# Kernel tuning notes

Measured on AMD Instinct MI355X. Metric: run time of the kernel, lower is better.

## Reference

```python
import jax, jax.numpy as jnp
import numpy as np

B, C, H, W = 2, 16, 128, 128
PS = (3, 5, 7)
N_BG, N_TG = 64, 8


def _unfold(x, p):
    # torch F.unfold(kernel=p, padding=p//2, stride=1): [B,C,H,W] -> [B, C*p*p, H*W]
    pad = p // 2
    b, c, h, w = x.shape
    xp = jnp.pad(x, ((0, 0), (0, 0), (pad, pad), (pad, pad)))
    # channel-major, then kernel row, kernel col (torch layout)
    pat = jnp.stack([xp[:, :, i:i + h, j:j + w] for i in range(p) for j in range(p)], axis=2)
    return pat.reshape(b, c * p * p, h * w)


def _fold(cols, p, h, w):
    # torch F.fold(output_size=(h,w), kernel=p, padding=p//2, stride=1): overlap-add scatter
    b, d, _ = cols.shape
    c = d // (p * p)
    pad = p // 2
    pat = cols.reshape(b, c, p * p, h, w)
    canvas = jnp.zeros((b, c, h + 2 * pad, w + 2 * pad), cols.dtype)
    for k in range(p * p):
        i, j = divmod(k, p)
        canvas = canvas.at[:, :, i:i + h, j:j + w].add(pat[:, :, k])
    return canvas[:, :, pad:pad + h, pad:pad + w]


def _branch(x, memory, temp, p):
    # _read_memory ('dot' similarity) + fold reconstruction with overlap-count divisor
    b, c, h, w = x.shape
    d = memory.shape[1]  # c*p*p
    xu = _unfold(x, p).transpose(0, 2, 1)                      # [B, HW, D]
    sim = jnp.einsum('bld,md->blm', xu, memory) * (temp[0] / d ** 0.5)
    att = jax.nn.softmax(sim, axis=2)                          # [B, HW, M]
    read = jnp.einsum('blm,md->bld', att, memory)              # [B, HW, D]
    out_sum = _fold(read.transpose(0, 2, 1), p, h, w)
    ones = jnp.ones((1, 1, h, w), x.dtype)
    div = _fold(_unfold(ones, p), p, h, w)                     # overlap counts
    return out_sum / (div + 1e-8)


def _fusion(feats, w1, b1, w2, b2):
    # MultiScaleFusion, fusion_type='attention'
    n = len(feats)
    b, c = feats[0].shape[0], feats[0].shape[1]
    u = feats[0]
    for f in feats[1:]:
        u = u + f
    pooled = u.mean(axis=(2, 3))                               # [B, C]
    hdn = jax.nn.relu(pooled @ w1.T + b1)                      # [B, C//4]
    logits = (hdn @ w2.T + b2).reshape(b, n, c)                # [B, n, C]
    wt = jax.nn.softmax(logits, axis=1)[..., None, None]       # softmax over scales
    return (jnp.stack(feats, axis=1) * wt).sum(axis=1)


def setup_inputs() -> dict:
    key = jax.random.key(0)
    ks = jax.random.split(key, 20)
    inp = {
        'bg': jax.random.normal(ks[0], (B, C, H, W), jnp.float32),
        'tg': jax.random.normal(ks[1], (B, C, H, W), jnp.float32),
    }
    for i, p in enumerate(PS):
        inp[f'bg_mem{i}'] = jax.random.normal(ks[2 + i], (N_BG, C * p * p), jnp.float32)
        inp[f'tg_mem{i}'] = jax.random.normal(ks[5 + i], (N_TG, C * p * p), jnp.float32)
        inp[f'bg_temp{i}'] = jnp.full((1,), 10.0, jnp.float32)
        inp[f'tg_temp{i}'] = jnp.full((1,), 10.0, jnp.float32)
    hid = C // 4
    n = len(PS)
    s1 = (1.0 / C) ** 0.5
    s2 = (1.0 / hid) ** 0.5
    inp['bg_fc1_w'] = jax.random.uniform(ks[8], (hid, C), jnp.float32, -s1, s1)
    inp['bg_fc1_b'] = jax.random.uniform(ks[9], (hid,), jnp.float32, -s1, s1)
    inp['bg_fc2_w'] = jax.random.uniform(ks[10], (C * n, hid), jnp.float32, -s2, s2)
    inp['bg_fc2_b'] = jax.random.uniform(ks[11], (C * n,), jnp.float32, -s2, s2)
    inp['tg_fc1_w'] = jax.random.uniform(ks[12], (hid, C), jnp.float32, -s1, s1)
    inp['tg_fc1_b'] = jax.random.uniform(ks[13], (hid,), jnp.float32, -s1, s1)
    inp['tg_fc2_w'] = jax.random.uniform(ks[14], (C * n, hid), jnp.float32, -s2, s2)
    inp['tg_fc2_b'] = jax.random.uniform(ks[15], (C * n,), jnp.float32, -s2, s2)
    return inp


def reference(bg, tg,
              bg_mem0, bg_mem1, bg_mem2, bg_temp0, bg_temp1, bg_temp2,
              tg_mem0, tg_mem1, tg_mem2, tg_temp0, tg_temp1, tg_temp2,
              bg_fc1_w, bg_fc1_b, bg_fc2_w, bg_fc2_b,
              tg_fc1_w, tg_fc1_b, tg_fc2_w, tg_fc2_b):
    bg_feats = [_branch(bg, m, t, p) for m, t, p in
                zip((bg_mem0, bg_mem1, bg_mem2), (bg_temp0, bg_temp1, bg_temp2), PS)]
    f_bc = _fusion(bg_feats, bg_fc1_w, bg_fc1_b, bg_fc2_w, bg_fc2_b)
    tg_feats = [_branch(tg, m, t, p) for m, t, p in
                zip((tg_mem0, tg_mem1, tg_mem2), (tg_temp0, tg_temp1, tg_temp2), PS)]
    f_tg = _fusion(tg_feats, tg_fc1_w, tg_fc1_b, tg_fc2_w, tg_fc2_b)
    return (f_bc, f_tg)
```

## Files before the change

### kernel.cpp

```cpp
#include <hip/hip_runtime.h>

#define C_CH 16
#define Hdim 128
#define Wdim 128
#define HWdim 16384
#define CHW (C_CH * HWdim)
#define Bdim 2
#define PAIR_ELEMS (Bdim * CHW)

#define XWP 140
#define XHP 140
#define XPL (XHP * XWP)

typedef float v2f __attribute__((ext_vector_type(2)));
typedef _Float16 h2 __attribute__((ext_vector_type(2)));
typedef _Float16 f16x8 __attribute__((ext_vector_type(8)));
typedef float f32x4 __attribute__((ext_vector_type(4)));

__device__ __forceinline__ unsigned pack2(float a, float b) {
  h2 h = {(_Float16)a, (_Float16)b};
  return __builtin_bit_cast(unsigned, h);
}
__device__ __forceinline__ void gadd(float* p, float v) {
  __hip_atomic_fetch_add(p, v, __ATOMIC_RELAXED, __HIP_MEMORY_SCOPE_AGENT);
}

struct PrepDesc {
  const float* mem;
  const float* temp;
  _Float16* simA;
  _Float16* readA;
  int M, D, P, tg;
};
struct PrepArgs { PrepDesc d[6]; };

__global__ __launch_bounds__(256) void k_prep(PrepArgs a) {
  PrepDesc de = a.d[blockIdx.y];
  int n = de.M * de.D;
  int idx = blockIdx.x * 256 + threadIdx.x;
  if (idx >= n) return;
  int m = idx / de.D;
  int d = idx - m * de.D;
  float val = de.mem[idx];
  float sc = de.temp[0] / sqrtf((float)de.D);
  int pp = de.P * de.P;
  int c = d / pp;
  int r = d - c * pp;
  int i = r / de.P;
  int j = r - i * de.P;
  int uv = i * de.P + j;
  int uvp = uv >> 1, luv = uv & 1;
  int kk = luv * 16 + c, kg = kk >> 3, kl = kk & 7;
  int u = de.P - 1 - i, v = de.P - 1 - j;
  int uvf = u * de.P + v;
  float sv = val * sc;
  if (!de.tg) {
    int mt = m >> 4, row = m & 15;
    _Float16 hi = (_Float16)sv;
    size_t bi = ((size_t)uvp * 8 + mt) * 512 + row * 32 +
                (size_t)((kg ^ (row & 3)) * 8 + kl);
    de.simA[bi] = hi;
    de.simA[bi + 2048] = (_Float16)(sv - (float)hi);
    int ck = m >> 5, m5 = m & 31, kg2 = m5 >> 3, kl2 = m5 & 7;
    _Float16 hr = (_Float16)val;
    size_t b2 = (size_t)uvf * 2048 + (size_t)(ck * 2) * 512 + c * 32 +
                (size_t)((kg2 ^ (c & 3)) * 8 + kl2);
    de.readA[b2] = hr;
    de.readA[b2 + 512] = (_Float16)(val - (float)hr);
  } else {
    _Float16 hi = (_Float16)sv;
    size_t bi = (size_t)(uvp * 2) * 512 + m * 32 +
                (size_t)((kg ^ (m & 3)) * 8 + kl);
    de.simA[bi] = hi;
    de.simA[bi + 512] = (_Float16)(sv - (float)hi);
    int ch = uvf >> 2, q = uvf & 3;
    _Float16 hr = (_Float16)val;
    size_t b2 = (size_t)ch * 1024 + c * 32 +
                (size_t)((q ^ (c & 3)) * 8 + (m & 7));
    de.readA[b2] = hr;
    de.readA[b2 + 512] = (_Float16)(val - (float)hr);
  }
}

__global__ __launch_bounds__(256) void k_padx(const float* __restrict__ bg,
                                              const float* __restrict__ tg,
                                              unsigned* __restrict__ xpad2)
{
  int idx = blockIdx.x * 256 + threadIdx.x;
  int pp = idx >> 14;
  int hw = idx & (HWdim - 1);
  int y = hw >> 7, x = hw & 127;
  int z = pp >> 3, cp = pp & 7;
  const float* src = (z < 2) ? bg : tg;
  int b = z & 1;
  float a = src[((b * C_CH + 2 * cp) << 14) + hw];
  float bb = src[((b * C_CH + 2 * cp + 1) << 14) + hw];
  xpad2[(size_t)pp * XPL + (y + 6) * XWP + (x + 6)] = pack2(a, bb);
}

struct FusedArgs {
  const unsigned* xpad2;
  const _Float16* simA[3];
  const _Float16* readA[3];
  const _Float16* simAtg[3];
  const _Float16* readAtg[3];
  float* fbgs[3];
  float* ftgs[3];
  float* pooled;
};

#define FX_ATT 17920
#define FX_ABUF 58880
#define FX_SMEM 75264

template<int P, bool BG>
__device__ __forceinline__ void fused_body(
    const unsigned* __restrict__ xp,
    const _Float16* __restrict__ simA,
    const _Float16* __restrict__ readA,
    float* __restrict__ fout,
    float* __restrict__ poolp,
    unsigned char* smem, int tid, int x0, int y0)
{
  constexpr int PAD = P / 2;
  constexpr int THY = 8 + 2 * PAD, THX = 16 + 2 * PAD;
  constexpr int XH = 8 + 4 * PAD, XW = 16 + 4 * PAD;
  constexpr int NXP = XH * XW, NHP = THY * THX;
  constexpr int NT = (NHP + 15) / 16;
  constexpr int NUVP = (P * P + 1) / 2;
  constexpr int NCH = BG ? (P * P + 1) / 2 : (P * P + 3) / 4;
  constexpr int NMT = BG ? 4 : 1;
  constexpr int SCHB = BG ? 8192 : 2048;
  constexpr int RCHB = BG ? 8192 : 2048;
  constexpr int SLD = SCHB / 16, RLD = RCHB / 16;
  constexpr int NRACC = BG ? 4 : 2;

  unsigned char* xbuf = smem;
  unsigned char* att  = smem + FX_ATT;
  unsigned char* abuf = smem + FX_ABUF;

  const int w = __builtin_amdgcn_readfirstlane(tid >> 6);
  const int lane = tid & 63;
  const int col = lane & 15, g = lane >> 4;

  const int oy = y0 - 2 * PAD + 6, ox = x0 - 2 * PAD + 6;
  for (int t = tid; t < 2 * NXP; t += 512) {
    int h = (t >= NXP) ? 1 : 0;
    int pix = t - h * NXP;
    int ly = pix / XW, lx = pix - ly * XW;
    const unsigned* s = xp + (size_t)(h * 4) * XPL + (oy + ly) * XWP + (ox + lx);
    uint4 vv = { s[0], s[XPL], s[2 * XPL], s[3 * XPL] };
    *(uint4*)(xbuf + (h * NXP + pix) * 16) = vv;
  }

  int ayv[3], axv[3];
#pragma unroll
  for (int ti = 0; ti < 3; ++ti) {
    int nt = w + ti * 8;
    int pix = nt * 16 + col;
    if (pix > NHP - 1) pix = NHP - 1;
    ayv[ti] = pix / THX;
    axv[ti] = pix - ayv[ti] * THX;
  }

  f32x4 acc[3][NMT];
#pragma unroll
  for (int ti = 0; ti < 3; ++ti)
#pragma unroll
    for (int mt = 0; mt < NMT; ++mt) acc[ti][mt] = (f32x4){0.f, 0.f, 0.f, 0.f};

  uint4 sreg;
  if (tid < SLD) sreg = *((const uint4*)simA + tid);
  for (int uvp = 0; uvp < NUVP; ++uvp) {
    if (tid < SLD) {
      *((uint4*)(abuf + (uvp & 1) * 8192) + tid) = sreg;
      if (uvp + 1 < NUVP)
        sreg = *((const uint4*)(simA + (size_t)(uvp + 1) * (SCHB / 2)) + tid);
    }
    __syncthreads();

    const unsigned char* ab = abuf + (uvp & 1) * 8192;
    f16x8 af[2][NMT];
#pragma unroll
    for (int s = 0; s < 2; ++s)
#pragma unroll
      for (int mt = 0; mt < NMT; ++mt)
        af[s][mt] = *(const f16x8*)(ab + (s * NMT + mt) * 1024 + col * 64 +
                                    ((g ^ (col & 3)) << 4));

    int uva = 2 * uvp;
    int uvb = uva + 1; if (uvb >= P * P) uvb = uva;
    const int ua = uva / P, va = uva - ua * P;
    const int ub = uvb / P, vb = uvb - ub * P;
    const int u_ = (g >= 2) ? ub : ua;
    const int v_ = (g >= 2) ? vb : va;

#pragma unroll
    for (int ti = 0; ti < 3; ++ti) {
      int nt = w + ti * 8;
      if (nt < NT) {
        int xpix = (ayv[ti] + u_) * XW + axv[ti] + v_;
        f16x8 bb = *(const f16x8*)(xbuf + ((g & 1) * NXP + xpix) * 16);
#pragma unroll
        for (int mt = 0; mt < NMT; ++mt) {
          acc[ti][mt] = __builtin_amdgcn_mfma_f32_16x16x32_f16(af[0][mt], bb, acc[ti][mt], 0, 0, 0);
          acc[ti][mt] = __builtin_amdgcn_mfma_f32_16x16x32_f16(af[1][mt], bb, acc[ti][mt], 0, 0, 0);
        }
      }
    }
  }

  uint4 rreg;
  if (tid < RLD) rreg = *((const uint4*)readA + tid);

#pragma unroll
  for (int ti = 0; ti < 3; ++ti) {
    int nt = w + ti * 8;
    if (nt < NT) {
      int pa = nt * 16 + col;
      int say = pa / THX, sax = pa - say * THX;
      int gy = y0 + say - PAD, gx = x0 + sax - PAD;
      bool inimg = (pa < NHP) & (gy >= 0) & (gy < Hdim) & (gx >= 0) & (gx < Wdim);
      if constexpr (BG) {
        float l[16];
#pragma unroll
        for (int mt = 0; mt < 4; ++mt)
#pragma unroll
          for (int r = 0; r < 4; ++r) l[mt * 4 + r] = acc[ti][mt][r];
        float mx = l[0];
#pragma unroll
        for (int i2 = 1; i2 < 16; ++i2) mx = fmaxf(mx, l[i2]);
        mx = fmaxf(mx, __shfl_xor(mx, 16));
        mx = fmaxf(mx, __shfl_xor(mx, 32));
        float sum = 0.f;
#pragma unroll
        for (int i2 = 0; i2 < 16; ++i2) { l[i2] = __expf(l[i2] - mx); sum += l[i2]; }
        sum += __shfl_xor(sum, 16);
        sum += __shfl_xor(sum, 32);
        float inv = inimg ? (1.f / sum) : 0.f;
        unsigned char* base = att + pa * 128;
        int swz = (pa & 7) << 4;
#pragma unroll
        for (int mt = 0; mt < 4; ++mt) {
          uint2 st = { pack2(l[mt * 4 + 0] * inv, l[mt * 4 + 1] * inv),
                       pack2(l[mt * 4 + 2] * inv, l[mt * 4 + 3] * inv) };
          *(uint2*)(base + ((mt * 32 + g * 8) ^ swz)) = st;
        }
      } else {
        float l0 = acc[ti][0][0], l1 = acc[ti][0][1];
        float l2 = acc[ti][0][2], l3 = acc[ti][0][3];
        float mx = fmaxf(fmaxf(l0, l1), fmaxf(l2, l3));
        mx = fmaxf(mx, __shfl_xor(mx, 16));
        l0 = __expf(l0 - mx); l1 = __expf(l1 - mx);
        l2 = __expf(l2 - mx); l3 = __expf(l3 - mx);
        float sum = l0 + l1 + l2 + l3;
        sum += __shfl_xor(sum, 16);
        float inv = inimg ? (1.f / sum) : 0.f;
        if (g < 2) {
          uint2 st = { pack2(l0 * inv, l1 * inv), pack2(l2 * inv, l3 * inv) };
          *(uint2*)(att + pa * 16 + g * 8) = st;
        }
      }
    }
  }
  __syncthreads();

  f32x4 racc[NRACC];
#pragma unroll
  for (int q = 0; q < NRACC; ++q) racc[q] = (f32x4){0.f, 0.f, 0.f, 0.f};

  for (int ch = 0; ch < NCH; ++ch) {
    if (tid < RLD) {
      *((uint4*)(abuf + (ch & 1) * 8192) + tid) = rreg;
      if (ch + 1 < NCH)
        rreg = *((const uint4*)(readA + (size_t)(ch + 1) * (RCHB / 2)) + tid);
    }
    __syncthreads();
    const unsigned char* ab = abuf + (ch & 1) * 8192;
    if constexpr (BG) {
#pragma unroll
      for (int l = 0; l < 2; ++l) {
        int uv = 2 * ch + l;
        int uvc = (uv > P * P - 1) ? (P * P - 1) : uv;
        int u = uvc / P, v = uvc - u * P;
        int pix = (w + u) * THX + (col + v);
        int swz = (pix & 7) << 4;
#pragma unroll
        for (int ck = 0; ck < 2; ++ck) {
          f16x8 bb = *(const f16x8*)(att + pix * 128 + ((ck * 64 + g * 16) ^ swz));
          f16x8 ah = *(const f16x8*)(ab + (l * 4 + ck * 2 + 0) * 1024 + col * 64 +
                                     ((g ^ (col & 3)) << 4));
          f16x8 al = *(const f16x8*)(ab + (l * 4 + ck * 2 + 1) * 1024 + col * 64 +
                                     ((g ^ (col & 3)) << 4));
          racc[ck * 2 + 0] = __builtin_amdgcn_mfma_f32_16x16x32_f16(ah, bb, racc[ck * 2 + 0], 0, 0, 0);
          racc[ck * 2 + 1] = __builtin_amdgcn_mfma_f32_16x16x32_f16(al, bb, racc[ck * 2 + 1], 0, 0, 0);
        }
      }
    } else {
      int uv = 4 * ch + g;
      if (uv > P * P - 1) uv = P * P - 1;
      int u = uv / P, v = uv - u * P;
      int pix = (w + u) * THX + (col + v);
      f16x8 bb = *(const f16x8*)(att + pix * 16);
      int aoff = col * 64 + ((g ^ (col & 3)) << 4);
      f16x8 ah = *(const f16x8*)(ab + aoff);
      f16x8 al = *(const f16x8*)(ab + 1024 + aoff);
      racc[0] = __builtin_amdgcn_mfma_f32_16x16x32_f16(ah, bb, racc[0], 0, 0, 0);
      racc[1] = __builtin_amdgcn_mfma_f32_16x16x32_f16(al, bb, racc[1], 0, 0, 0);
    }
  }

  f32x4 sv;
  if constexpr (BG) sv = (racc[0] + racc[1]) + (racc[2] + racc[3]);
  else              sv = racc[0] + racc[1];
  int gy = y0 + w, gx = x0 + col;
  int cy = min(P - 1, gy + PAD) - max(0, gy + PAD - (Hdim - 1)) + 1;
  int cx = min(P - 1, gx + PAD) - max(0, gx + PAD - (Wdim - 1)) + 1;
  float inv = 1.f / ((float)(cy * cx) + 1e-8f);
  float o0 = sv[0] * inv, o1 = sv[1] * inv, o2 = sv[2] * inv, o3 = sv[3] * inv;
  float* outp = fout + (size_t)(g * 4) * HWdim + gy * Wdim + gx;
  outp[0] = o0;
  outp[(size_t)1 * HWdim] = o1;
  outp[(size_t)2 * HWdim] = o2;
  outp[(size_t)3 * HWdim] = o3;

  __syncthreads();
  *(f32x4*)(abuf + tid * 16) = (f32x4){o0, o1, o2, o3};
  __syncthreads();
  if (tid < 16) {
    const float* ap = (const float*)abuf;
    float sum = 0.f;
    for (int px = 0; px < 128; ++px) {
      int u = (px >> 4) * 64 + (tid >> 2) * 16 + (px & 15);
      sum += ap[u * 4 + (tid & 3)];
    }
    gadd(poolp + tid, sum * (1.0f / (float)HWdim));
  }
}

__global__ __launch_bounds__(512, 4) void k_fused(FusedArgs a) {
  __shared__ __align__(16) unsigned char smem[FX_SMEM];
  const int z = blockIdx.z;
  const int x0 = blockIdx.x * 16, y0 = blockIdx.y * 8;
  const int tid = threadIdx.x;
  if (z < 6) {
    const int si = z >> 1, b = z & 1;
    const unsigned* xp = a.xpad2 + (size_t)(b * 8) * XPL;
    float* pp = a.pooled + b * 16;
    if (si == 0)
      fused_body<7, true>(xp, a.simA[0], a.readA[0], a.fbgs[0] + (size_t)b * CHW, pp, smem, tid, x0, y0);
    else if (si == 1)
      fused_body<5, true>(xp, a.simA[1], a.readA[1], a.fbgs[1] + (size_t)b * CHW, pp, smem, tid, x0, y0);
    else
      fused_body<3, true>(xp, a.simA[2], a.readA[2], a.fbgs[2] + (size_t)b * CHW, pp, smem, tid, x0, y0);
  } else {
    const int zz = z - 6, si = zz >> 1, b = zz & 1;
    const unsigned* xp = a.xpad2 + (size_t)((2 + b) * 8) * XPL;
    float* pp = a.pooled + 32 + b * 16;
    if (si == 0)
      fused_body<7, false>(xp, a.simAtg[0], a.readAtg[0], a.ftgs[0] + (size_t)b * CHW, pp, smem, tid, x0, y0);
    else if (si == 1)
      fused_body<5, false>(xp, a.simAtg[1], a.readAtg[1], a.ftgs[1] + (size_t)b * CHW, pp, smem, tid, x0, y0);
    else
      fused_body<3, false>(xp, a.simAtg[2], a.readAtg[2], a.ftgs[2] + (size_t)b * CHW, pp, smem, tid, x0, y0);
  }
}

__global__ __launch_bounds__(128) void k_mlp(
    const float* __restrict__ pooled,
    const float* __restrict__ w1b, const float* __restrict__ b1b,
    const float* __restrict__ w2b, const float* __restrict__ b2b,
    const float* __restrict__ w1t, const float* __restrict__ b1t,
    const float* __restrict__ w2t, const float* __restrict__ b2t,
    float* __restrict__ wt)
{
  __shared__ float hdn[Bdim][4];
  __shared__ float lg[Bdim][48];
  int t = threadIdx.x;
  for (int br = 0; br < 2; ++br) {
    const float* w1 = br ? w1t : w1b;
    const float* b1 = br ? b1t : b1b;
    const float* w2 = br ? w2t : w2b;
    const float* b2 = br ? b2t : b2b;
    if (t < 8) {
      int b = t >> 2, h = t & 3;
      float s = b1[h];
      for (int c = 0; c < C_CH; ++c) s += pooled[br * 32 + b * 16 + c] * w1[h * 16 + c];
      hdn[b][h] = fmaxf(s, 0.f);
    }
    __syncthreads();
    if (t < 96) {
      int b = t / 48, j = t - b * 48;
      float s = b2[j];
      for (int h = 0; h < 4; ++h) s += hdn[b][h] * w2[j * 4 + h];
      lg[b][j] = s;
    }
    __syncthreads();
    if (t < 32) {
      int b = t >> 4, c = t & 15;
      float l0 = lg[b][c], l1 = lg[b][16 + c], l2 = lg[b][32 + c];
      float m = fmaxf(l0, fmaxf(l1, l2));
      float e0 = __expf(l0 - m), e1 = __expf(l1 - m), e2 = __expf(l2 - m);
      float inv = 1.f / (e0 + e1 + e2);
      wt[((br * 2 + b) * 3 + 0) * 16 + c] = e0 * inv;
      wt[((br * 2 + b) * 3 + 1) * 16 + c] = e1 * inv;
      wt[((br * 2 + b) * 3 + 2) * 16 + c] = e2 * inv;
    }
    __syncthreads();
  }
}

__global__ __launch_bounds__(256) void k_out(const float* __restrict__ fbg,
                                             const float* __restrict__ ftg,
                                             const float* __restrict__ wt,
                                             float* __restrict__ out)
{
  int idx = blockIdx.x * 256 + threadIdx.x;
  int br  = idx >> 19;
  int rem = idx & ((1 << 19) - 1);
  int b   = rem >> 18;
  int off = rem & ((1 << 18) - 1);
  int c   = off >> 14;
  const float* f = (br == 0) ? fbg : ftg;
  int wbase = (br * 2 + b) * 3;
  float acc = 0.f;
#pragma unroll
  for (int s = 0; s < 3; ++s) {
    float v = f[(size_t)(s * 2 + b) * CHW + off];
    acc = fmaf(wt[(wbase + s) * 16 + c], v, acc);
  }
  out[idx] = acc;
}

extern "C" void kernel_launch(void* const* d_in, const int* in_sizes, int n_in,
                              void* d_out, int out_size, void* d_ws, size_t ws_size,
                              hipStream_t stream)
{
  const float* bg = (const float*)d_in[0];
  const float* tg = (const float*)d_in[1];
  const float* bg_mem[3]  = {(const float*)d_in[2],  (const float*)d_in[6],  (const float*)d_in[10]};
  const float* tg_mem[3]  = {(const float*)d_in[3],  (const float*)d_in[7],  (const float*)d_in[11]};
  const float* bg_temp[3] = {(const float*)d_in[4],  (const float*)d_in[8],  (const float*)d_in[12]};
  const float* tg_temp[3] = {(const float*)d_in[5],  (const float*)d_in[9],  (const float*)d_in[13]};
  const float* bg_fc1_w = (const float*)d_in[14];
  const float* bg_fc1_b = (const float*)d_in[15];
  const float* bg_fc2_w = (const float*)d_in[16];
  const float* bg_fc2_b = (const float*)d_in[17];
  const float* tg_fc1_w = (const float*)d_in[18];
  const float* tg_fc1_b = (const float*)d_in[19];
  const float* tg_fc2_w = (const float*)d_in[20];
  const float* tg_fc2_b = (const float*)d_in[21];

  unsigned* ws = (unsigned*)d_ws;
  unsigned* xpad2   = ws;
  float*    pooled  = (float*)(ws + (size_t)32 * XPL);
  float*    wt      = pooled + 64;
  _Float16* simA    = (_Float16*)(wt + 192);
  _Float16* readA   = simA + 176128;
  _Float16* simAtg  = readA + 176128;
  _Float16* readAtg = simAtg + 44032;
  float*    ftg     = (float*)(readAtg + 23552);
  float*    fbg     = ftg + (size_t)6 * CHW;

  hipMemsetAsync(xpad2, 0, (size_t)837376 * 4, stream);

  const int   Ms[6] = {64, 64, 64, 8, 8, 8};
  const int   Ps[6] = {3, 5, 7, 3, 5, 7};
  const float* mems[6]  = {bg_mem[0], bg_mem[1], bg_mem[2], tg_mem[0], tg_mem[1], tg_mem[2]};
  const float* temps[6] = {bg_temp[0], bg_temp[1], bg_temp[2], tg_temp[0], tg_temp[1], tg_temp[2]};

  const size_t aOff[3]   = {0, 102400, 155648};
  const size_t sOffTg[3] = {0, 25600, 38912};
  const size_t rOffTg[3] = {0, 13312, 20480};

  PrepArgs pa;
  for (int k = 0; k < 6; ++k) {
    int D = C_CH * Ps[k] * Ps[k];
    int si = 2 - (k % 3);
    if (k < 3)
      pa.d[k] = {mems[k], temps[k], simA + aOff[si], readA + aOff[si],
                 Ms[k], D, Ps[k], 0};
    else
      pa.d[k] = {mems[k], temps[k], simAtg + sOffTg[si], readAtg + rOffTg[si],
                 Ms[k], D, Ps[k], 1};
  }
  k_prep<<<dim3(196, 6), 256, 0, stream>>>(pa);
  k_padx<<<2048, 256, 0, stream>>>(bg, tg, xpad2);

  FusedArgs fa;
  fa.xpad2 = xpad2;
  fa.pooled = pooled;
  for (int si = 0; si < 3; ++si) {
    int p = 2 - si;
    fa.simA[si]    = simA + aOff[si];
    fa.readA[si]   = readA + aOff[si];
    fa.simAtg[si]  = simAtg + sOffTg[si];
    fa.readAtg[si] = readAtg + rOffTg[si];
    fa.fbgs[si]    = fbg + (size_t)p * 2 * CHW;
    fa.ftgs[si]    = ftg + (size_t)p * 2 * CHW;
  }

  k_fused<<<dim3(8, 16, 12), 512, 0, stream>>>(fa);

  k_mlp<<<1, 128, 0, stream>>>(pooled, bg_fc1_w, bg_fc1_b, bg_fc2_w, bg_fc2_b,
                               tg_fc1_w, tg_fc1_b, tg_fc2_w, tg_fc2_b, wt);
  k_out<<<(2 * PAIR_ELEMS) / 256, 256, 0, stream>>>(fbg, ftg, wt, (float*)d_out);
}
```

Measured before the change: 177.0 us.

## Shrink fused-kernel LDS footprint for higher occupancy and merge prep/pad launches

```diff
diff --git a/kernel.cpp b/kernel.cpp
--- a/kernel.cpp
+++ b/kernel.cpp
@@ -34,10 +34,30 @@
 };
 struct PrepArgs { PrepDesc d[6]; };
 
-__global__ __launch_bounds__(256) void k_prep(PrepArgs a) {
-  PrepDesc de = a.d[blockIdx.y];
+__global__ __launch_bounds__(256) void k_preppad(PrepArgs a,
+                                                 const float* __restrict__ bg,
+                                                 const float* __restrict__ tg,
+                                                 unsigned* __restrict__ xpad2)
+{
+  int bid = blockIdx.x;
+  if (bid < 2048) {
+    int idx = bid * 256 + threadIdx.x;
+    int pp = idx >> 14;
+    int hw = idx & (HWdim - 1);
+    int y = hw >> 7, x = hw & 127;
+    int z = pp >> 3, cp = pp & 7;
+    const float* src = (z < 2) ? bg : tg;
+    int b = z & 1;
+    float av = src[((b * C_CH + 2 * cp) << 14) + hw];
+    float bv = src[((b * C_CH + 2 * cp + 1) << 14) + hw];
+    xpad2[(size_t)pp * XPL + (y + 6) * XWP + (x + 6)] = pack2(av, bv);
+    return;
+  }
+  int p = bid - 2048;
+  int gy = p / 196, gx = p - gy * 196;
+  PrepDesc de = a.d[gy];
   int n = de.M * de.D;
-  int idx = blockIdx.x * 256 + threadIdx.x;
+  int idx = gx * 256 + threadIdx.x;
   if (idx >= n) return;
   int m = idx / de.D;
   int d = idx - m * de.D;
@@ -82,22 +102,6 @@
   }
 }
 
-__global__ __launch_bounds__(256) void k_padx(const float* __restrict__ bg,
-                                              const float* __restrict__ tg,
-                                              unsigned* __restrict__ xpad2)
-{
-  int idx = blockIdx.x * 256 + threadIdx.x;
-  int pp = idx >> 14;
-  int hw = idx & (HWdim - 1);
-  int y = hw >> 7, x = hw & 127;
-  int z = pp >> 3, cp = pp & 7;
-  const float* src = (z < 2) ? bg : tg;
-  int b = z & 1;
-  float a = src[((b * C_CH + 2 * cp) << 14) + hw];
-  float bb = src[((b * C_CH + 2 * cp + 1) << 14) + hw];
-  xpad2[(size_t)pp * XPL + (y + 6) * XWP + (x + 6)] = pack2(a, bb);
-}
-
 struct FusedArgs {
   const unsigned* xpad2;
   const _Float16* simA[3];
@@ -109,9 +113,9 @@
   float* pooled;
 };
 
-#define FX_ATT 17920
-#define FX_ABUF 58880
-#define FX_SMEM 75264
+#define SDB_OFF 17920
+#define RBUF_OFF 40960
+#define FX_SMEM 49152
 
 template<int P, bool BG>
 __device__ __forceinline__ void fused_body(
@@ -136,8 +140,9 @@
   constexpr int NRACC = BG ? 4 : 2;
 
   unsigned char* xbuf = smem;
-  unsigned char* att  = smem + FX_ATT;
-  unsigned char* abuf = smem + FX_ABUF;
+  unsigned char* att  = smem;
+  unsigned char* sdb  = smem + SDB_OFF;
+  unsigned char* rbuf = smem + RBUF_OFF;
 
   const int w = __builtin_amdgcn_readfirstlane(tid >> 6);
   const int lane = tid & 63;
@@ -173,13 +178,13 @@
   if (tid < SLD) sreg = *((const uint4*)simA + tid);
   for (int uvp = 0; uvp < NUVP; ++uvp) {
     if (tid < SLD) {
-      *((uint4*)(abuf + (uvp & 1) * 8192) + tid) = sreg;
+      *((uint4*)(sdb + (uvp & 1) * SCHB) + tid) = sreg;
       if (uvp + 1 < NUVP)
         sreg = *((const uint4*)(simA + (size_t)(uvp + 1) * (SCHB / 2)) + tid);
     }
     __syncthreads();
 
-    const unsigned char* ab = abuf + (uvp & 1) * 8192;
+    const unsigned char* ab = sdb + (uvp & 1) * SCHB;
     f16x8 af[2][NMT];
 #pragma unroll
     for (int s = 0; s < 2; ++s)
@@ -212,6 +217,7 @@
 
   uint4 rreg;
   if (tid < RLD) rreg = *((const uint4*)readA + tid);
+  __syncthreads();
 
 #pragma unroll
   for (int ti = 0; ti < 3; ++ti) {
@@ -263,20 +269,20 @@
       }
     }
   }
-  __syncthreads();
 
   f32x4 racc[NRACC];
 #pragma unroll
   for (int q = 0; q < NRACC; ++q) racc[q] = (f32x4){0.f, 0.f, 0.f, 0.f};
 
   for (int ch = 0; ch < NCH; ++ch) {
+    __syncthreads();
     if (tid < RLD) {
-      *((uint4*)(abuf + (ch & 1) * 8192) + tid) = rreg;
+      *((uint4*)rbuf + tid) = rreg;
       if (ch + 1 < NCH)
         rreg = *((const uint4*)(readA + (size_t)(ch + 1) * (RCHB / 2)) + tid);
     }
     __syncthreads();
-    const unsigned char* ab = abuf + (ch & 1) * 8192;
+    const unsigned char* ab = rbuf;
     if constexpr (BG) {
 #pragma unroll
       for (int l = 0; l < 2; ++l) {
@@ -324,21 +330,32 @@
   outp[(size_t)2 * HWdim] = o2;
   outp[(size_t)3 * HWdim] = o3;
 
+  float s0 = o0, s1 = o1, s2 = o2, s3 = o3;
+#pragma unroll
+  for (int mask = 1; mask < 16; mask <<= 1) {
+    s0 += __shfl_xor(s0, mask);
+    s1 += __shfl_xor(s1, mask);
+    s2 += __shfl_xor(s2, mask);
+    s3 += __shfl_xor(s3, mask);
+  }
   __syncthreads();
-  *(f32x4*)(abuf + tid * 16) = (f32x4){o0, o1, o2, o3};
+  float* red = (float*)rbuf;
+  if (col == 0) {
+    red[(w * 4 + g) * 4 + 0] = s0;
+    red[(w * 4 + g) * 4 + 1] = s1;
+    red[(w * 4 + g) * 4 + 2] = s2;
+    red[(w * 4 + g) * 4 + 3] = s3;
+  }
   __syncthreads();
   if (tid < 16) {
-    const float* ap = (const float*)abuf;
-    float sum = 0.f;
-    for (int px = 0; px < 128; ++px) {
-      int u = (px >> 4) * 64 + (tid >> 2) * 16 + (px & 15);
-      sum += ap[u * 4 + (tid & 3)];
-    }
-    gadd(poolp + tid, sum * (1.0f / (float)HWdim));
-  }
-}
-
-__global__ __launch_bounds__(512, 4) void k_fused(FusedArgs a) {
+    float t = 0.f;
+#pragma unroll
+    for (int ww = 0; ww < 8; ++ww) t += red[ww * 16 + tid];
+    gadd(poolp + tid, t * (1.0f / (float)HWdim));
+  }
+}
+
+__global__ __launch_bounds__(512, 6) void k_fused(FusedArgs a) {
   __shared__ __align__(16) unsigned char smem[FX_SMEM];
   const int z = blockIdx.z;
   const int x0 = blockIdx.x * 16, y0 = blockIdx.y * 8;
@@ -484,8 +501,7 @@
       pa.d[k] = {mems[k], temps[k], simAtg + sOffTg[si], readAtg + rOffTg[si],
                  Ms[k], D, Ps[k], 1};
   }
-  k_prep<<<dim3(196, 6), 256, 0, stream>>>(pa);
-  k_padx<<<2048, 256, 0, stream>>>(bg, tg, xpad2);
+  k_preppad<<<3224, 256, 0, stream>>>(pa, bg, tg, xpad2);
 
   FusedArgs fa;
   fa.xpad2 = xpad2;
```

Result: slower. 219.6 us (+24.1%).
